# Optimization experiments

Hardware: AMD Instinct MI355X
Metric: run time of the kernel (lower is better)

Reference implementation:

```python
import jax, jax.numpy as jnp
import numpy as np

B, S, DIM = 1, 2048, 4096
N_HEADS, N_KV_HEADS = 32, 8
HEAD_DIM = DIM // N_HEADS            # 128
N_REP = N_HEADS // N_KV_HEADS        # 4
Q_SIZE = N_HEADS * HEAD_DIM          # 4096
KV_SIZE = N_KV_HEADS * HEAD_DIM      # 1024


def setup_inputs() -> dict:
    key = jax.random.key(0)
    ks = jax.random.split(key, 5)
    x = jax.random.normal(ks[0], (B, S, DIM), dtype=jnp.float32)
    # RoPE tables: freqs_cis[s, j] = exp(i * s * theta_j), theta_j = 10000^(-2j/head_dim)
    theta = 10000.0 ** (-jnp.arange(0, HEAD_DIM, 2, dtype=jnp.float32) / HEAD_DIM)
    ang = jnp.arange(S, dtype=jnp.float32)[:, None] * theta[None, :]  # [S, HEAD_DIM//2]
    freqs_cos = jnp.cos(ang)
    freqs_sin = jnp.sin(ang)
    # causal additive mask [1,1,S,S]
    causal = jnp.tril(jnp.ones((S, S), dtype=bool))
    mask = jnp.where(causal, 0.0, -1e9).astype(jnp.float32)[None, None]
    wqkv = jax.random.normal(ks[1], (Q_SIZE + 2 * KV_SIZE, DIM), dtype=jnp.float32) * (DIM ** -0.5)
    wo = jax.random.normal(ks[2], (DIM, Q_SIZE), dtype=jnp.float32) * (Q_SIZE ** -0.5)
    return {"x": x, "freqs_cos": freqs_cos, "freqs_sin": freqs_sin, "mask": mask,
            "wqkv": wqkv, "wo": wo}


def _apply_rope(t, cos, sin):
    # t: [B, S, H, D]; cos/sin: [S, D//2]  (complex multiply on (even, odd) pairs)
    b, s, h, d = t.shape
    tp = t.reshape(b, s, h, d // 2, 2)
    t0, t1 = tp[..., 0], tp[..., 1]
    c = cos[None, :, None, :]
    sn = sin[None, :, None, :]
    out = jnp.stack([t0 * c - t1 * sn, t0 * sn + t1 * c], axis=-1)
    return out.reshape(b, s, h, d)


def reference(x, freqs_cos, freqs_sin, mask, wqkv, wo):
    bsz, seqlen, _ = x.shape
    qkv = jnp.einsum('bsd,od->bso', x, wqkv)  # fused QKV projection
    xq = qkv[..., :Q_SIZE].reshape(bsz, seqlen, N_HEADS, HEAD_DIM)
    xk = qkv[..., Q_SIZE:Q_SIZE + KV_SIZE].reshape(bsz, seqlen, N_KV_HEADS, HEAD_DIM)
    xv = qkv[..., Q_SIZE + KV_SIZE:].reshape(bsz, seqlen, N_KV_HEADS, HEAD_DIM)
    # rotary embedding on q, k
    xq = _apply_rope(xq, freqs_cos, freqs_sin)
    xk = _apply_rope(xk, freqs_cos, freqs_sin)
    # cache insertion (prefill: cache == current k/v), layout [B, KVH, S, D]
    cache_k = jnp.swapaxes(xk, 1, 2)
    cache_v = jnp.swapaxes(xv, 1, 2)
    # GQA repeat_kv -> [B, H, S, D]
    keys = jnp.repeat(cache_k, N_REP, axis=1)
    values = jnp.repeat(cache_v, N_REP, axis=1)
    # scores: einsum 'ijkl,ikml->ikjm' with xq [b,s,h,d], keys [b,h,t,d] -> [b,h,s,t]
    scores = jnp.einsum('bshd,bhtd->bhst', xq, keys) / jnp.sqrt(jnp.float32(HEAD_DIM))
    scores = scores + mask
    scores = jax.nn.softmax(scores.astype(jnp.float32), axis=-1).astype(xq.dtype)
    out = jnp.einsum('bhst,bhtd->bhsd', scores, values)  # [B, H, S, D]
    out = jnp.swapaxes(out, 1, 2).reshape(bsz, seqlen, Q_SIZE)
    return jnp.einsum('bso,do->bsd', out, wo)
```

## Files before the change

### kernel.cpp

```cpp
#include <hip/hip_runtime.h>
#include <hip/hip_bf16.h>
#include <cstdint>
#include <cstddef>


typedef __attribute__((ext_vector_type(4)))  float    f32x4;
typedef __attribute__((ext_vector_type(16))) float    f32x16;
typedef __attribute__((ext_vector_type(8)))  __bf16   bf16x8;
typedef __attribute__((ext_vector_type(4)))  __bf16   bf16x4;
typedef __attribute__((ext_vector_type(2)))  __bf16   bf16x2;
typedef __attribute__((ext_vector_type(4)))  uint32_t u32x4;

typedef const __attribute__((address_space(1))) void* gaddr_t;
typedef __attribute__((address_space(3))) void*       laddr_t;

#define S_LEN   2048
#define DIM_    4096
#define NH      32
#define NKV     8
#define HD      128
#define QKV_LD  6144
#define KOFF    4096
#define VOFF    5120

#define EXP2F(x) __builtin_amdgcn_exp2f(x)

__global__ void cvt_f32_bf16(const float* __restrict__ in, __bf16* __restrict__ out, int n4) {
  int idx = blockIdx.x * blockDim.x + threadIdx.x;
  int stride = gridDim.x * blockDim.x;
  for (int i = idx; i < n4; i += stride) {
    float4 v = reinterpret_cast<const float4*>(in)[i];
    bf16x4 o;
    o[0] = (__bf16)v.x; o[1] = (__bf16)v.y; o[2] = (__bf16)v.z; o[3] = (__bf16)v.w;
    reinterpret_cast<bf16x4*>(out)[i] = o;
  }
}

__global__ void rope_kernel(__bf16* __restrict__ qkv, const float* __restrict__ fc,
                            const float* __restrict__ fs) {
  int tid = blockIdx.x * 256 + threadIdx.x;
  int i = tid & 63;
  int t = tid >> 6;
  int h = t % 40;
  int s = t / 40;
  int col = (h < NH) ? (h * HD + 2 * i) : (KOFF + (h - NH) * HD + 2 * i);
  size_t off = (size_t)s * QKV_LD + col;
  float c = fc[s * 64 + i], sn = fs[s * 64 + i];
  bf16x2 v = *reinterpret_cast<bf16x2*>(&qkv[off]);
  float t0 = (float)v[0], t1 = (float)v[1];
  bf16x2 o;
  o[0] = (__bf16)(t0 * c - t1 * sn);
  o[1] = (__bf16)(t0 * sn + t1 * c);
  *reinterpret_cast<bf16x2*>(&qkv[off]) = o;
}

__device__ __forceinline__ void stage128(const __bf16* __restrict__ P, int ld, int row0,
                                         int kt, char* dst, int tid) {
#pragma unroll
  for (int j = 0; j < 2; ++j) {
    int c = j * 512 + tid;
    int r = c >> 3, g = c & 7;
    const __bf16* src = P + (size_t)(row0 + r) * ld + kt * 64 + ((g ^ (r & 7)) * 8);
    __builtin_amdgcn_global_load_lds((gaddr_t)src,
        (laddr_t)(dst + j * 8192 + (tid & ~63) * 16), 16, 0, 0);
  }
}

template <int BM, int Q, bool DOVM>
__device__ __forceinline__ void gphase(const __bf16* Ab, const __bf16* Bb,
                                       f32x4 (&acc)[BM / 32][4],
                                       int wm, int wn, int l15, int hi4, int tid,
                                       bool s0, bool s1, const __bf16* __restrict__ P, int ld,
                                       int row0a, char* dsta, int row0b, char* dstb, int kt) {
  constexpr int MFR = BM / 64;
  constexpr int QM = Q >> 1, QN = Q & 1;
  bf16x8 af[MFR][2], bf_[2][2];
#pragma unroll
  for (int mi = 0; mi < MFR; ++mi) {
    int R = wm * (BM / 2) + QM * (BM / 4) + mi * 16 + l15;
#pragma unroll
    for (int kk = 0; kk < 2; ++kk)
      af[mi][kk] = *reinterpret_cast<const bf16x8*>(
          (const char*)Ab + R * 128 + (((kk * 4 + hi4) ^ (R & 7)) * 16));
  }
#pragma unroll
  for (int ni = 0; ni < 2; ++ni) {
    int R = wn * 64 + QN * 32 + ni * 16 + l15;
#pragma unroll
    for (int kk = 0; kk < 2; ++kk)
      bf_[ni][kk] = *reinterpret_cast<const bf16x8*>(
          (const char*)Bb + R * 128 + (((kk * 4 + hi4) ^ (R & 7)) * 16));
  }
  if (s0) stage128(P, ld, row0a, kt, dsta, tid);
  if (s1) stage128(P, ld, row0b, kt, dstb, tid);
  __builtin_amdgcn_s_barrier();
  asm volatile("s_waitcnt lgkmcnt(0)" ::: "memory");
  __builtin_amdgcn_sched_barrier(0);
  __builtin_amdgcn_s_setprio(1);
#pragma unroll
  for (int mi = 0; mi < MFR; ++mi)
#pragma unroll
    for (int ni = 0; ni < 2; ++ni)
#pragma unroll
      for (int kk = 0; kk < 2; ++kk)
        acc[QM * MFR + mi][QN * 2 + ni] = __builtin_amdgcn_mfma_f32_16x16x32_bf16(
            af[mi][kk], bf_[ni][kk], acc[QM * MFR + mi][QN * 2 + ni], 0, 0, 0);
  __builtin_amdgcn_s_setprio(0);
  if (DOVM) asm volatile("s_waitcnt vmcnt(0)" ::: "memory");
  __builtin_amdgcn_s_barrier();
}

template <int BM, typename OutT>
__global__ __launch_bounds__(512, 2) void gemm_bt8(const __bf16* __restrict__ A,
                                                   const __bf16* __restrict__ B,
                                                   OutT* __restrict__ C, int K,
                                                   int lda, int ldb, int ldc, int nbx) {
  __shared__ __align__(16) __bf16 As[2][BM * 64];
  __shared__ __align__(16) __bf16 Bs[2][256 * 64];
  const int tid = threadIdx.x;
  const int l15 = tid & 15, hi4 = (tid >> 4) & 3, w = tid >> 6;
  const int wm = w >> 2, wn = w & 3;
  const int cpx = gridDim.x >> 3;
  const int id2 = ((int)blockIdx.x & 7) * cpx + ((int)blockIdx.x >> 3);
  const int m0 = (id2 / nbx) * BM, n0 = (id2 % nbx) * 256;

  f32x4 acc[BM / 32][4] = {};

  stage128(A, lda, m0, 0, (char*)As[0], tid);
  if constexpr (BM == 256) stage128(A, lda, m0 + 128, 0, (char*)As[0] + 16384, tid);
  stage128(B, ldb, n0, 0, (char*)Bs[0], tid);
  stage128(B, ldb, n0 + 128, 0, (char*)Bs[0] + 16384, tid);
  asm volatile("s_waitcnt vmcnt(0)" ::: "memory");
  __builtin_amdgcn_s_barrier();

  const int ntiles = K >> 6;
  for (int it = 0; it < ntiles; it += 2) {
    const int t1 = it + 1, t2 = it + 2;
    const bool more = t2 < ntiles;
    gphase<BM, 0, false>(As[0], Bs[0], acc, wm, wn, l15, hi4, tid,
                         true, BM == 256, A, lda, m0, (char*)As[1], m0 + 128, (char*)As[1] + 16384, t1);
    gphase<BM, 1, false>(As[0], Bs[0], acc, wm, wn, l15, hi4, tid,
                         true, true, B, ldb, n0, (char*)Bs[1], n0 + 128, (char*)Bs[1] + 16384, t1);
    gphase<BM, 2, false>(As[0], Bs[0], acc, wm, wn, l15, hi4, tid,
                         false, false, A, lda, 0, (char*)As[1], 0, (char*)As[1], t1);
    gphase<BM, 3, true >(As[0], Bs[0], acc, wm, wn, l15, hi4, tid,
                         false, false, A, lda, 0, (char*)As[1], 0, (char*)As[1], t1);
    gphase<BM, 0, false>(As[1], Bs[1], acc, wm, wn, l15, hi4, tid,
                         more, more && BM == 256, A, lda, m0, (char*)As[0], m0 + 128, (char*)As[0] + 16384, t2);
    gphase<BM, 1, false>(As[1], Bs[1], acc, wm, wn, l15, hi4, tid,
                         more, more, B, ldb, n0, (char*)Bs[0], n0 + 128, (char*)Bs[0] + 16384, t2);
    gphase<BM, 2, false>(As[1], Bs[1], acc, wm, wn, l15, hi4, tid,
                         false, false, A, lda, 0, (char*)As[0], 0, (char*)As[0], t2);
    gphase<BM, 3, true >(As[1], Bs[1], acc, wm, wn, l15, hi4, tid,
                         false, false, A, lda, 0, (char*)As[0], 0, (char*)As[0], t2);
  }

#pragma unroll
  for (int MI = 0; MI < BM / 32; ++MI)
#pragma unroll
    for (int NI = 0; NI < 4; ++NI)
#pragma unroll
      for (int j = 0; j < 4; ++j) {
        int row = m0 + wm * (BM / 2) + MI * 16 + hi4 * 4 + j;
        int col = n0 + wn * 64 + NI * 16 + l15;
        C[(size_t)row * ldc + col] = (OutT)acc[MI][NI][j];
      }
}

__device__ inline uint32_t pack2(float a, float b) {
  bf16x2 t; t[0] = (__bf16)a; t[1] = (__bf16)b;
  return __builtin_bit_cast(uint32_t, t);
}

__global__ __launch_bounds__(256, 2) void attn_kernel(const __bf16* __restrict__ qkv,
                                                      __bf16* __restrict__ out) {
  __shared__ __align__(16) __bf16 Ks[2][64 * 128];
  __shared__ __align__(16) __bf16 Vt[2][128][72];
  const int tid = threadIdx.x;
  const int lane = tid & 63, l31 = lane & 31, hi = lane >> 5, wq = tid >> 6;
  const int head = blockIdx.x & 31;
  const int pr = blockIdx.x >> 5;
  const int kvh = head >> 2;
  const float sc2 = 0.08838834764831845f * 1.44269504089f;

  bf16x8 vr[2][2];

  auto stage_k = [&](int tt, int buf) {
#pragma unroll
    for (int i = 0; i < 4; ++i) {
      int c = i * 256 + tid;
      int r = c >> 4, g = c & 15;
      const __bf16* gk = qkv + (size_t)(tt * 64 + r) * QKV_LD + KOFF + kvh * HD + ((g ^ (r & 7)) * 8);
      __builtin_amdgcn_global_load_lds((gaddr_t)gk,
          (laddr_t)((char*)Ks[buf] + (tid & ~63) * 16 + i * 4096), 16, 0, 0);
    }
  };
  auto load_v = [&](int tt) {
#pragma unroll
    for (int i = 0; i < 2; ++i) {
      int task = i * 256 + tid;
      int p = task >> 4, cg = task & 15;
      const __bf16* vp = qkv + (size_t)(tt * 64 + 2 * p) * QKV_LD + VOFF + kvh * HD + cg * 8;
      vr[i][0] = *reinterpret_cast<const bf16x8*>(vp);
      vr[i][1] = *reinterpret_cast<const bf16x8*>(vp + QKV_LD);
    }
  };
  auto write_v = [&](int buf) {
#pragma unroll
    for (int i = 0; i < 2; ++i) {
      int task = i * 256 + tid;
      int p = task >> 4, cg = task & 15;
#pragma unroll
      for (int e0 = 0; e0 < 8; ++e0) {
        int e = e0 ^ (lane & 7);
        bf16x2 pkv; pkv[0] = vr[i][0][e]; pkv[1] = vr[i][1][e];
        *reinterpret_cast<bf16x2*>(&Vt[buf][cg * 8 + e][2 * p]) = pkv;
      }
    }
  };

  for (int pass = 0; pass < 2; ++pass) {
    const int qt = pass ? (15 - pr) : pr;
    const int q0 = qt * 128;
    const int nt = 2 * qt + 2;
    const int qr = q0 + wq * 32 + l31;

    bf16x8 qf[8];
    {
      const __bf16* qp = qkv + (size_t)qr * QKV_LD + head * HD + hi * 8;
#pragma unroll
      for (int ks = 0; ks < 8; ++ks) qf[ks] = *reinterpret_cast<const bf16x8*>(qp + ks * 16);
    }
    f32x16 o[4] = {};
    float m_run = -3e38f, l_run = 0.f;

    __syncthreads();
    stage_k(0, 0); load_v(0); write_v(0);

    for (int t = 0; t < nt; ++t) {
      const int cur = t & 1;
      __syncthreads();
      if (t + 1 < nt) { stage_k(t + 1, 1 - cur); load_v(t + 1); }

      f32x16 st[2];
#pragma unroll
      for (int sub = 0; sub < 2; ++sub) {
        f32x16 acc = {};
        int r = sub * 32 + l31;
#pragma unroll
        for (int ks = 0; ks < 8; ++ks) {
          int g = (ks * 2 + hi) ^ (r & 7);
          bf16x8 kf = *reinterpret_cast<const bf16x8*>((char*)Ks[cur] + r * 256 + g * 16);
          acc = __builtin_amdgcn_mfma_f32_32x32x16_bf16(kf, qf[ks], acc, 0, 0, 0);
        }
        st[sub] = acc;
      }
#pragma unroll
      for (int sub = 0; sub < 2; ++sub)
#pragma unroll
        for (int e = 0; e < 16; ++e) st[sub][e] *= sc2;
      if (t >= nt - 2) {
        const int kv0 = t * 64;
#pragma unroll
        for (int sub = 0; sub < 2; ++sub)
#pragma unroll
          for (int e = 0; e < 16; ++e) {
            int kvg = kv0 + sub * 32 + (e & 3) + 8 * (e >> 2) + 4 * hi;
            if (kvg > qr) st[sub][e] = -1e30f;
          }
      }
      float pm = st[0][0];
#pragma unroll
      for (int e = 1; e < 16; ++e) pm = fmaxf(pm, st[0][e]);
#pragma unroll
      for (int e = 0; e < 16; ++e) pm = fmaxf(pm, st[1][e]);
      pm = fmaxf(pm, __shfl_xor(pm, 32));
      if (!__all(pm - m_run <= 8.f)) {
        float mn = fmaxf(m_run, pm);
        float fsc = EXP2F(m_run - mn);
        m_run = mn;
        l_run *= fsc;
#pragma unroll
        for (int dt = 0; dt < 4; ++dt)
#pragma unroll
          for (int e = 0; e < 16; ++e) o[dt][e] *= fsc;
      }
      float rs = 0.f;
#pragma unroll
      for (int sub = 0; sub < 2; ++sub)
#pragma unroll
        for (int e = 0; e < 16; ++e) {
          float p = EXP2F(st[sub][e] - m_run);
          st[sub][e] = p;
          rs += p;
        }
      rs += __shfl_xor(rs, 32);
      l_run += rs;

      uint32_t pk[16];
#pragma unroll
      for (int sub = 0; sub < 2; ++sub)
#pragma unroll
        for (int i = 0; i < 8; ++i)
          pk[sub * 8 + i] = pack2(st[sub][2 * i], st[sub][2 * i + 1]);
      uint32_t rv[8];
#pragma unroll
      for (int m = 0; m < 8; ++m) {
        int base = 4 * (m >> 1) + (m & 1);
        uint32_t snd = hi ? pk[base] : pk[base + 2];
        rv[m] = __shfl_xor(snd, 32);
      }
      bf16x8 pf[4];
#pragma unroll
      for (int tt = 0; tt < 4; ++tt) {
        u32x4 w;
        w[0] = hi ? rv[2 * tt]     : pk[4 * tt];
        w[1] = hi ? rv[2 * tt + 1] : pk[4 * tt + 1];
        w[2] = hi ? pk[4 * tt + 2] : rv[2 * tt];
        w[3] = hi ? pk[4 * tt + 3] : rv[2 * tt + 1];
        pf[tt] = __builtin_bit_cast(bf16x8, w);
      }
#pragma unroll
      for (int dt = 0; dt < 4; ++dt) {
        int dr = dt * 32 + l31;
#pragma unroll
        for (int tt = 0; tt < 4; ++tt) {
          bf16x8 vf = *reinterpret_cast<const bf16x8*>((char*)&Vt[cur][0][0] + dr * 144 + tt * 32 + hi * 16);
          o[dt] = __builtin_amdgcn_mfma_f32_32x32x16_bf16(vf, pf[tt], o[dt], 0, 0, 0);
        }
      }
      if (t + 1 < nt) write_v(1 - cur);
    }

    float inv = 1.f / l_run;
    __bf16* scr = &Ks[0][0] + wq * 1280;
    const int qq = lane >> 1, part = lane & 1;
#pragma unroll
    for (int dt = 0; dt < 4; ++dt) {
      __syncthreads();
#pragma unroll
      for (int i = 0; i < 8; ++i) {
        int d0 = (2 * i & 3) + 8 * (i >> 1) + 4 * hi;
        bf16x2 prr;
        prr[0] = (__bf16)(o[dt][2 * i] * inv);
        prr[1] = (__bf16)(o[dt][2 * i + 1] * inv);
        *reinterpret_cast<bf16x2*>(scr + l31 * 40 + d0) = prr;
      }
      __syncthreads();
      bf16x8 r0 = *reinterpret_cast<const bf16x8*>(scr + qq * 40 + part * 16);
      bf16x8 r1 = *reinterpret_cast<const bf16x8*>(scr + qq * 40 + part * 16 + 8);
      __bf16* op = out + (size_t)(q0 + wq * 32 + qq) * DIM_ + head * HD + dt * 32 + part * 16;
      *reinterpret_cast<bf16x8*>(op) = r0;
      *reinterpret_cast<bf16x8*>(op + 8) = r1;
    }
  }
}

extern "C" void kernel_launch(void* const* d_in, const int* in_sizes, int n_in,
                              void* d_out, int out_size, void* d_ws, size_t ws_size,
                              hipStream_t stream) {
  (void)in_sizes; (void)n_in; (void)out_size; (void)ws_size;
  const float* x    = (const float*)d_in[0];
  const float* fc   = (const float*)d_in[1];
  const float* fs   = (const float*)d_in[2];
  const float* wqkv = (const float*)d_in[4];
  const float* wo   = (const float*)d_in[5];
  float* out = (float*)d_out;

  char* ws = (char*)d_ws;
  __bf16* xb    = (__bf16*)(ws);
  __bf16* wqkvb = (__bf16*)(ws + 16777216);
  __bf16* wob   = (__bf16*)(ws + 67108864);
  __bf16* qkv   = (__bf16*)(ws + 100663296);
  __bf16* attnO = xb;

  cvt_f32_bf16<<<2048, 256, 0, stream>>>(x,    xb,    (S_LEN * DIM_) / 4);
  cvt_f32_bf16<<<2048, 256, 0, stream>>>(wqkv, wqkvb, (6144 * DIM_) / 4);
  cvt_f32_bf16<<<2048, 256, 0, stream>>>(wo,   wob,   (DIM_ * DIM_) / 4);

  gemm_bt8<256, __bf16><<<192, 512, 0, stream>>>(xb, wqkvb, qkv, DIM_, DIM_, DIM_, QKV_LD, 24);

  rope_kernel<<<(S_LEN * 40 * 64) / 256, 256, 0, stream>>>(qkv, fc, fs);

  attn_kernel<<<256, 256, 0, stream>>>(qkv, attnO);

  gemm_bt8<128, float><<<256, 512, 0, stream>>>(attnO, wob, out, DIM_, DIM_, DIM_, DIM_, 16);
}
```

Measured before the change: 394.2 us.

## Retile QKV GEMM to 256x192 for full-CU grid and restructure k-phase pipeline

```diff
diff --git a/kernel.cpp b/kernel.cpp
--- a/kernel.cpp
+++ b/kernel.cpp
@@ -54,115 +54,107 @@
   *reinterpret_cast<bf16x2*>(&qkv[off]) = o;
 }
 
-__device__ __forceinline__ void stage128(const __bf16* __restrict__ P, int ld, int row0,
-                                         int kt, char* dst, int tid) {
-#pragma unroll
-  for (int j = 0; j < 2; ++j) {
-    int c = j * 512 + tid;
-    int r = c >> 3, g = c & 7;
-    const __bf16* src = P + (size_t)(row0 + r) * ld + kt * 64 + ((g ^ (r & 7)) * 8);
-    __builtin_amdgcn_global_load_lds((gaddr_t)src,
-        (laddr_t)(dst + j * 8192 + (tid & ~63) * 16), 16, 0, 0);
-  }
-}
-
-template <int BM, int Q, bool DOVM>
-__device__ __forceinline__ void gphase(const __bf16* Ab, const __bf16* Bb,
-                                       f32x4 (&acc)[BM / 32][4],
+__device__ __forceinline__ void stage64(const __bf16* __restrict__ P, int ld, int row0,
+                                        int kt, char* dst, int tid) {
+  int r = tid >> 3, g = tid & 7;
+  const __bf16* src = P + (size_t)(row0 + r) * ld + kt * 64 + ((g ^ (r & 7)) * 8);
+  __builtin_amdgcn_global_load_lds((gaddr_t)src,
+      (laddr_t)(dst + (tid & ~63) * 16), 16, 0, 0);
+}
+
+template <int BM, int BN, int QM, int QK, bool ST, bool VM>
+__device__ __forceinline__ void phase8(const __bf16* Ab, const __bf16* Bb,
+                                       f32x4 (&acc)[BM / 32][BN / 64],
                                        int wm, int wn, int l15, int hi4, int tid,
-                                       bool s0, bool s1, const __bf16* __restrict__ P, int ld,
-                                       int row0a, char* dsta, int row0b, char* dstb, int kt) {
-  constexpr int MFR = BM / 64;
-  constexpr int QM = Q >> 1, QN = Q & 1;
-  bf16x8 af[MFR][2], bf_[2][2];
-#pragma unroll
-  for (int mi = 0; mi < MFR; ++mi) {
+                                       const __bf16* __restrict__ A, int lda, int m0, char* dA,
+                                       const __bf16* __restrict__ B, int ldb, int n0, char* dB,
+                                       int kt) {
+  constexpr int MH = BM / 64;
+  constexpr int NI = BN / 64;
+  bf16x8 af[MH], bfr[NI];
+#pragma unroll
+  for (int mi = 0; mi < MH; ++mi) {
     int R = wm * (BM / 2) + QM * (BM / 4) + mi * 16 + l15;
-#pragma unroll
-    for (int kk = 0; kk < 2; ++kk)
-      af[mi][kk] = *reinterpret_cast<const bf16x8*>(
-          (const char*)Ab + R * 128 + (((kk * 4 + hi4) ^ (R & 7)) * 16));
-  }
-#pragma unroll
-  for (int ni = 0; ni < 2; ++ni) {
-    int R = wn * 64 + QN * 32 + ni * 16 + l15;
-#pragma unroll
-    for (int kk = 0; kk < 2; ++kk)
-      bf_[ni][kk] = *reinterpret_cast<const bf16x8*>(
-          (const char*)Bb + R * 128 + (((kk * 4 + hi4) ^ (R & 7)) * 16));
-  }
-  if (s0) stage128(P, ld, row0a, kt, dsta, tid);
-  if (s1) stage128(P, ld, row0b, kt, dstb, tid);
+    af[mi] = *reinterpret_cast<const bf16x8*>(
+        (const char*)Ab + R * 128 + (((QK * 4 + hi4) ^ (R & 7)) * 16));
+  }
+#pragma unroll
+  for (int ni = 0; ni < NI; ++ni) {
+    int R = wn * (BN / 4) + ni * 16 + l15;
+    bfr[ni] = *reinterpret_cast<const bf16x8*>(
+        (const char*)Bb + R * 128 + (((QK * 4 + hi4) ^ (R & 7)) * 16));
+  }
+  if (ST) {
+#pragma unroll
+    for (int h = 0; h < BM / 64; ++h) stage64(A, lda, m0 + h * 64, kt, dA + h * 8192, tid);
+#pragma unroll
+    for (int h = 0; h < BN / 64; ++h) stage64(B, ldb, n0 + h * 64, kt, dB + h * 8192, tid);
+  }
   __builtin_amdgcn_s_barrier();
   asm volatile("s_waitcnt lgkmcnt(0)" ::: "memory");
   __builtin_amdgcn_sched_barrier(0);
   __builtin_amdgcn_s_setprio(1);
 #pragma unroll
-  for (int mi = 0; mi < MFR; ++mi)
-#pragma unroll
-    for (int ni = 0; ni < 2; ++ni)
-#pragma unroll
-      for (int kk = 0; kk < 2; ++kk)
-        acc[QM * MFR + mi][QN * 2 + ni] = __builtin_amdgcn_mfma_f32_16x16x32_bf16(
-            af[mi][kk], bf_[ni][kk], acc[QM * MFR + mi][QN * 2 + ni], 0, 0, 0);
+  for (int mi = 0; mi < MH; ++mi)
+#pragma unroll
+    for (int ni = 0; ni < NI; ++ni)
+      acc[QM * MH + mi][ni] = __builtin_amdgcn_mfma_f32_16x16x32_bf16(
+          af[mi], bfr[ni], acc[QM * MH + mi][ni], 0, 0, 0);
   __builtin_amdgcn_s_setprio(0);
-  if (DOVM) asm volatile("s_waitcnt vmcnt(0)" ::: "memory");
+  if (VM) asm volatile("s_waitcnt vmcnt(0)" ::: "memory");
   __builtin_amdgcn_s_barrier();
 }
 
-template <int BM, typename OutT>
-__global__ __launch_bounds__(512, 2) void gemm_bt8(const __bf16* __restrict__ A,
-                                                   const __bf16* __restrict__ B,
-                                                   OutT* __restrict__ C, int K,
-                                                   int lda, int ldb, int ldc, int nbx) {
-  __shared__ __align__(16) __bf16 As[2][BM * 64];
-  __shared__ __align__(16) __bf16 Bs[2][256 * 64];
+template <int BM, int BN, typename OutT>
+__global__ __launch_bounds__(512, 2) void gemm8(const __bf16* __restrict__ A,
+                                                const __bf16* __restrict__ B,
+                                                OutT* __restrict__ C, int K,
+                                                int lda, int ldb, int ldc,
+                                                int sx, int mxn) {
+  constexpr int ASZ = BM * 64, BSZ = BN * 64;
+  __shared__ __align__(16) __bf16 As[2][ASZ];
+  __shared__ __align__(16) __bf16 Bs[2][BSZ];
   const int tid = threadIdx.x;
   const int l15 = tid & 15, hi4 = (tid >> 4) & 3, w = tid >> 6;
   const int wm = w >> 2, wn = w & 3;
-  const int cpx = gridDim.x >> 3;
-  const int id2 = ((int)blockIdx.x & 7) * cpx + ((int)blockIdx.x >> 3);
-  const int m0 = (id2 / nbx) * BM, n0 = (id2 % nbx) * 256;
-
-  f32x4 acc[BM / 32][4] = {};
-
-  stage128(A, lda, m0, 0, (char*)As[0], tid);
-  if constexpr (BM == 256) stage128(A, lda, m0 + 128, 0, (char*)As[0] + 16384, tid);
-  stage128(B, ldb, n0, 0, (char*)Bs[0], tid);
-  stage128(B, ldb, n0 + 128, 0, (char*)Bs[0] + 16384, tid);
+  const int bid = blockIdx.x, xcd = bid & 7, lid = bid >> 3;
+  const int cm = (xcd >> sx) * 4 + (lid >> 3);
+  const int cn = (xcd & mxn) * 8 + (lid & 7);
+  const int m0 = cm * BM, n0 = cn * BN;
+
+  f32x4 acc[BM / 32][BN / 64] = {};
+
+#pragma unroll
+  for (int h = 0; h < BM / 64; ++h) stage64(A, lda, m0 + h * 64, 0, (char*)As[0] + h * 8192, tid);
+#pragma unroll
+  for (int h = 0; h < BN / 64; ++h) stage64(B, ldb, n0 + h * 64, 0, (char*)Bs[0] + h * 8192, tid);
   asm volatile("s_waitcnt vmcnt(0)" ::: "memory");
   __builtin_amdgcn_s_barrier();
 
   const int ntiles = K >> 6;
-  for (int it = 0; it < ntiles; it += 2) {
-    const int t1 = it + 1, t2 = it + 2;
-    const bool more = t2 < ntiles;
-    gphase<BM, 0, false>(As[0], Bs[0], acc, wm, wn, l15, hi4, tid,
-                         true, BM == 256, A, lda, m0, (char*)As[1], m0 + 128, (char*)As[1] + 16384, t1);
-    gphase<BM, 1, false>(As[0], Bs[0], acc, wm, wn, l15, hi4, tid,
-                         true, true, B, ldb, n0, (char*)Bs[1], n0 + 128, (char*)Bs[1] + 16384, t1);
-    gphase<BM, 2, false>(As[0], Bs[0], acc, wm, wn, l15, hi4, tid,
-                         false, false, A, lda, 0, (char*)As[1], 0, (char*)As[1], t1);
-    gphase<BM, 3, true >(As[0], Bs[0], acc, wm, wn, l15, hi4, tid,
-                         false, false, A, lda, 0, (char*)As[1], 0, (char*)As[1], t1);
-    gphase<BM, 0, false>(As[1], Bs[1], acc, wm, wn, l15, hi4, tid,
-                         more, more && BM == 256, A, lda, m0, (char*)As[0], m0 + 128, (char*)As[0] + 16384, t2);
-    gphase<BM, 1, false>(As[1], Bs[1], acc, wm, wn, l15, hi4, tid,
-                         more, more, B, ldb, n0, (char*)Bs[0], n0 + 128, (char*)Bs[0] + 16384, t2);
-    gphase<BM, 2, false>(As[1], Bs[1], acc, wm, wn, l15, hi4, tid,
-                         false, false, A, lda, 0, (char*)As[0], 0, (char*)As[0], t2);
-    gphase<BM, 3, true >(As[1], Bs[1], acc, wm, wn, l15, hi4, tid,
-                         false, false, A, lda, 0, (char*)As[0], 0, (char*)As[0], t2);
+  for (int t = 0; t < ntiles; ++t) {
+    const int cur = t & 1;
+    const __bf16* Ab = As[cur];
+    const __bf16* Bb = Bs[cur];
+    char* dA = (char*)As[1 - cur];
+    char* dB = (char*)Bs[1 - cur];
+    if (t + 1 < ntiles)
+      phase8<BM, BN, 0, 0, true,  false>(Ab, Bb, acc, wm, wn, l15, hi4, tid, A, lda, m0, dA, B, ldb, n0, dB, t + 1);
+    else
+      phase8<BM, BN, 0, 0, false, false>(Ab, Bb, acc, wm, wn, l15, hi4, tid, A, lda, m0, dA, B, ldb, n0, dB, 0);
+    phase8<BM, BN, 0, 1, false, false>(Ab, Bb, acc, wm, wn, l15, hi4, tid, A, lda, m0, dA, B, ldb, n0, dB, 0);
+    phase8<BM, BN, 1, 0, false, false>(Ab, Bb, acc, wm, wn, l15, hi4, tid, A, lda, m0, dA, B, ldb, n0, dB, 0);
+    phase8<BM, BN, 1, 1, false, true >(Ab, Bb, acc, wm, wn, l15, hi4, tid, A, lda, m0, dA, B, ldb, n0, dB, 0);
   }
 
 #pragma unroll
   for (int MI = 0; MI < BM / 32; ++MI)
 #pragma unroll
-    for (int NI = 0; NI < 4; ++NI)
+    for (int NI = 0; NI < BN / 64; ++NI)
 #pragma unroll
       for (int j = 0; j < 4; ++j) {
         int row = m0 + wm * (BM / 2) + MI * 16 + hi4 * 4 + j;
-        int col = n0 + wn * 64 + NI * 16 + l15;
+        int col = n0 + wn * (BN / 4) + NI * 16 + l15;
         C[(size_t)row * ldc + col] = (OutT)acc[MI][NI][j];
       }
 }
@@ -378,11 +370,11 @@
   cvt_f32_bf16<<<2048, 256, 0, stream>>>(wqkv, wqkvb, (6144 * DIM_) / 4);
   cvt_f32_bf16<<<2048, 256, 0, stream>>>(wo,   wob,   (DIM_ * DIM_) / 4);
 
-  gemm_bt8<256, __bf16><<<192, 512, 0, stream>>>(xb, wqkvb, qkv, DIM_, DIM_, DIM_, QKV_LD, 24);
+  gemm8<256, 192, __bf16><<<256, 512, 0, stream>>>(xb, wqkvb, qkv, DIM_, DIM_, DIM_, QKV_LD, 2, 3);
 
   rope_kernel<<<(S_LEN * 40 * 64) / 256, 256, 0, stream>>>(qkv, fc, fs);
 
   attn_kernel<<<256, 256, 0, stream>>>(qkv, attnO);
 
-  gemm_bt8<128, float><<<256, 512, 0, stream>>>(attnO, wob, out, DIM_, DIM_, DIM_, DIM_, 16);
-}
+  gemm8<128, 256, float><<<256, 512, 0, stream>>>(attnO, wob, out, DIM_, DIM_, DIM_, DIM_, 1, 1);
+}
```

Result: faster. 383.6 us (-2.7%).
